# Performance work log

Measured on AMD Instinct MI355X. Metric: run time of the kernel, lower is better.

Reference implementation:

```python
import jax, jax.numpy as jnp
import numpy as np

LATENT_PACKET_SIZE = 16

def setup_inputs() -> dict:
    key = jax.random.key(0)
    z = jax.random.normal(key, (4096, 1, 8192), dtype=jnp.float32)
    return {"z": z}

def reference(z) -> jnp.ndarray:
    B = z.shape[0]
    D = z.shape[2]
    P = LATENT_PACKET_SIZE
    n_packets = D // P
    zp = z.reshape(B, n_packets, P)                      # (B, N, P)
    # sort packets within each sample by the first element of each packet
    inds = jnp.argsort(zp[:, :, 0], axis=1)              # (B, N) int
    z_ordered = jnp.take_along_axis(zp, inds[:, :, None], axis=1)  # batched gather
    return z_ordered.reshape(B, 1, n_packets * P)
```

## Files before the change

kernel.cpp:

```cpp
#include <hip/hip_runtime.h>


#define NPK 512
#define DIM 8192
#define NT  512

__device__ __forceinline__ int swz(int e) { return e ^ ((e >> 3) & 7); }

__global__ __launch_bounds__(NT, 8)
void sort_latent_kernel(const float* __restrict__ z, float* __restrict__ out) {
    __shared__ float4 row4[DIM / 4];
    __shared__ __align__(16) unsigned long long keys[NPK];
    __shared__ int srcs[NPK];

    const int t = threadIdx.x;
    const size_t rowoff = (size_t)blockIdx.x * DIM;
    const float4* __restrict__ zin4 = (const float4*)(z + rowoff);
    float4* __restrict__ out4 = (float4*)(out + rowoff);

#pragma unroll
    for (int i = 0; i < DIM / 4 / NT; ++i) {
        const int e = t + NT * i;
        const float4 v = zin4[e];
        row4[swz(e)] = v;
        if ((t & 3) == 0) {
            const int p = (t >> 2) + (NT / 4) * i;
            unsigned int u = __float_as_uint(v.x);
            if (u == 0x80000000u) u = 0u;
            u = (u & 0x80000000u) ? ~u : (u | 0x80000000u);
            keys[p] = ((unsigned long long)u << 16) | (unsigned long long)p;
        }
    }
    __syncthreads();

    const unsigned long long k0 = keys[t];
    const ulonglong2* kv = (const ulonglong2*)keys;
    int r0 = 0;
#pragma unroll 8
    for (int j = 0; j < NPK / 2; j += 2) {
        const ulonglong2 a = kv[j];
        const ulonglong2 b = kv[j + 1];
        r0 += (int)(a.x < k0) + (int)(a.y < k0)
            + (int)(b.x < k0) + (int)(b.y < k0);
    }
    srcs[r0] = t;
    __syncthreads();

#pragma unroll
    for (int i = 0; i < DIM / 4 / NT; ++i) {
        const int o = t + NT * i;
        const int src = srcs[o >> 2];
        out4[o] = row4[swz((src << 2) | (o & 3))];
    }
}

extern "C" void kernel_launch(void* const* d_in, const int* in_sizes, int n_in,
                              void* d_out, int out_size, void* d_ws, size_t ws_size,
                              hipStream_t stream) {
    const float* z = (const float*)d_in[0];
    float* out = (float*)d_out;
    const int nrows = in_sizes[0] / DIM;
    sort_latent_kernel<<<nrows, NT, 0, stream>>>(z, out);
}
```

Before: 243.9 us.

## Replace O(N^2) rank-counting sort with bitonic sort using wave shuffles

Swaps the per-thread rank computation, where each thread compares its key against all 512 keys in shared memory, for a bitonic sorting network across the 512 threads. Exchange steps within a 64-lane wavefront use shuffle-xor on the two 32-bit halves of each key, and longer strides go through shared memory with barriers. This cuts the comparison work from 512 per thread to 45 compare-exchange steps, at the cost of extra barriers and shuffle latency on a kernel that may be dominated by memory traffic.

```diff
diff --git a/kernel.cpp b/kernel.cpp
--- a/kernel.cpp
+++ b/kernel.cpp
@@ -6,6 +6,12 @@
 #define NT  512
 
 __device__ __forceinline__ int swz(int e) { return e ^ ((e >> 3) & 7); }
+
+__device__ __forceinline__ unsigned long long shfl_xor_u64(unsigned long long v, int mask) {
+    const int lo = __shfl_xor((int)(unsigned int)(v & 0xffffffffull), mask);
+    const int hi = __shfl_xor((int)(unsigned int)(v >> 32), mask);
+    return ((unsigned long long)(unsigned int)hi << 32) | (unsigned int)lo;
+}
 
 __global__ __launch_bounds__(NT, 8)
 void sort_latent_kernel(const float* __restrict__ z, float* __restrict__ out) {
@@ -33,17 +39,30 @@
     }
     __syncthreads();
 
-    const unsigned long long k0 = keys[t];
-    const ulonglong2* kv = (const ulonglong2*)keys;
-    int r0 = 0;
-#pragma unroll 8
-    for (int j = 0; j < NPK / 2; j += 2) {
-        const ulonglong2 a = kv[j];
-        const ulonglong2 b = kv[j + 1];
-        r0 += (int)(a.x < k0) + (int)(a.y < k0)
-            + (int)(b.x < k0) + (int)(b.y < k0);
+    unsigned long long v = keys[t];
+
+#pragma unroll
+    for (int kk = 1; kk <= 9; ++kk) {
+        const int k = 1 << kk;
+#pragma unroll
+        for (int jj = kk - 1; jj >= 0; --jj) {
+            const int j = 1 << jj;
+            unsigned long long vp;
+            if (j < 64) {
+                vp = shfl_xor_u64(v, j);
+            } else {
+                __syncthreads();
+                keys[t] = v;
+                __syncthreads();
+                vp = keys[t ^ j];
+            }
+            const bool take_min = (((t & k) == 0) == ((t & j) == 0));
+            const bool lt = (v < vp);
+            v = (take_min == lt) ? v : vp;
+        }
     }
-    srcs[r0] = t;
+
+    srcs[t] = (int)(v & 0xffffull);
     __syncthreads();
 
 #pragma unroll
```

After: 235.7 us. 1.03x faster.
